# Optimization experiments

Measured on AMD Instinct MI355X. Metric: run time of the kernel, lower is better.

Reference implementation:

```python
import jax, jax.numpy as jnp
import numpy as np


def setup_inputs() -> dict:
    key = jax.random.key(0)
    B, H = 8192, 32768
    x = jax.random.normal(key, (B, H), dtype=jnp.float32)
    return {"hidden_preactivation_BH": x, "k": 64}


def reference(hidden_preactivation_BH, k):
    # top-k along last dim, then scatter values back into a zero tensor
    vals_BK, idx_BK = jax.lax.top_k(hidden_preactivation_BH, k)
    B = hidden_preactivation_BH.shape[0]
    rows_B1 = jnp.arange(B)[:, None]
    out_BH = jnp.zeros_like(hidden_preactivation_BH)
    out_BH = out_BH.at[rows_B1, idx_BK].set(vals_BK)
    return out_BH
```

## Files before the change

### kernel.cpp

```cpp
#include <hip/hip_runtime.h>
#include <stdint.h>

#define TPB 1024
#define NJ 8
#define HSZ 32768
#define NW (TPB / 64)
#define CAP 2048

__device__ __forceinline__ uint32_t f2k(float f) {
    uint32_t u = __float_as_uint(f);
    return u ^ (0x80000000u | (uint32_t)(-(int32_t)(u >> 31)));
}
__device__ __forceinline__ float k2f(uint32_t key) {
    uint32_t u = (key & 0x80000000u) ? (key ^ 0x80000000u) : ~key;
    return __uint_as_float(u);
}

__device__ __forceinline__ void select4096(const uint32_t* hist, uint32_t need,
                                           uint32_t* wtot, uint32_t* sh_bin,
                                           uint32_t* sh_rem, int t) {
    const int lane = t & 63, wid = t >> 6;
    uint32_t b[4], pt = 0;
#pragma unroll
    for (int jj = 0; jj < 4; ++jj) { b[jj] = hist[t * 4 + jj]; pt += b[jj]; }
    uint32_t pre = pt;
#pragma unroll
    for (int off = 1; off < 64; off <<= 1) {
        uint32_t n = (uint32_t)__shfl_down((int)pre, off, 64);
        if (lane + off < 64) pre += n;
    }
    if (lane == 0) wtot[wid] = pre;
    __syncthreads();
    uint32_t wsuf = 0;
    for (int w = wid + 1; w < NW; ++w) wsuf += wtot[w];
    const uint32_t Sincl = pre + wsuf;
    const uint32_t Sexcl = Sincl - pt;
    if (Sexcl < need && Sincl >= need) {
        uint32_t run = Sexcl;
#pragma unroll
        for (int jj = 3; jj >= 0; --jj) {
            if (run + b[jj] >= need) { *sh_bin = (uint32_t)(t * 4 + jj); *sh_rem = need - run; break; }
            run += b[jj];
        }
    }
    __syncthreads();
}

__device__ __forceinline__ void select256(const uint32_t* hist, uint32_t need,
                                          uint32_t* wtot, uint32_t* sh_bin,
                                          uint32_t* sh_rem, uint32_t* sh_eqcnt, int t) {
    const int lane = t & 63, wid = t >> 6;
    uint32_t pt = (t < 256) ? hist[t] : 0u;
    uint32_t pre = pt;
#pragma unroll
    for (int off = 1; off < 64; off <<= 1) {
        uint32_t n = (uint32_t)__shfl_down((int)pre, off, 64);
        if (lane + off < 64) pre += n;
    }
    if (lane == 0) wtot[wid] = pre;
    __syncthreads();
    uint32_t wsuf = 0;
    for (int w = wid + 1; w < NW; ++w) wsuf += wtot[w];
    const uint32_t Sincl = pre + wsuf;
    const uint32_t Sexcl = Sincl - pt;
    if (t < 256 && Sexcl < need && Sincl >= need) {
        *sh_bin = (uint32_t)t; *sh_rem = need - Sexcl; *sh_eqcnt = pt;
    }
    __syncthreads();
}

__global__ __launch_bounds__(TPB, 4) void topk_scatter_kernel(
    const float* __restrict__ x,
    const int* __restrict__ kp,
    float* __restrict__ out)
{
    __shared__ uint32_t hist[4096];
    __shared__ uint32_t wtot[NW];
    __shared__ uint32_t cand_key[CAP];
    __shared__ uint32_t cand_col[CAP];
    __shared__ uint32_t sh_bin, sh_rem, sh_eqcnt, sh_ncand;
    __shared__ uint32_t chunk_base;

    const int t = threadIdx.x;
    const size_t row = blockIdx.x;
    const float4* xr4 = reinterpret_cast<const float4*>(x + row * (size_t)HSZ);
    float* outr = out + row * (size_t)HSZ;
    float4* outr4 = reinterpret_cast<float4*>(outr);
    const uint32_t k = (uint32_t)kp[0];

    if (k == 0u || k >= (uint32_t)HSZ) {
#pragma unroll
        for (int j = 0; j < NJ; ++j) {
            float4 o;
            if (k == 0u) { o.x = o.y = o.z = o.w = 0.0f; }
            else o = xr4[j * TPB + t];
            outr4[j * TPB + t] = o;
        }
        return;
    }

    float4 vv[NJ];
#pragma unroll
    for (int j = 0; j < NJ; ++j) vv[j] = xr4[j * TPB + t];

    for (int i = t; i < 4096; i += TPB) hist[i] = 0u;
    if (t == 0) sh_ncand = 0u;
    __syncthreads();
#pragma unroll
    for (int j = 0; j < NJ; ++j) {
        atomicAdd(&hist[f2k(vv[j].x) >> 20], 1u);
        atomicAdd(&hist[f2k(vv[j].y) >> 20], 1u);
        atomicAdd(&hist[f2k(vv[j].z) >> 20], 1u);
        atomicAdd(&hist[f2k(vv[j].w) >> 20], 1u);
    }
    __syncthreads();
    select4096(hist, k, wtot, &sh_bin, &sh_rem, t);
    const uint32_t B1 = sh_bin;
    const uint32_t need2 = sh_rem;

#pragma unroll
    for (int j = 0; j < NJ; ++j) {
        float vals[4] = { vv[j].x, vv[j].y, vv[j].z, vv[j].w };
        float ov[4];
#pragma unroll
        for (int c = 0; c < 4; ++c) {
            uint32_t key = f2k(vals[c]);
            uint32_t b = key >> 20;
            ov[c] = (b > B1) ? vals[c] : 0.0f;
            if (b == B1) {
                uint32_t pos = atomicAdd(&sh_ncand, 1u);
                if (pos < CAP) {
                    cand_key[pos] = key;
                    cand_col[pos] = (uint32_t)((j * TPB + t) * 4 + c);
                }
            }
        }
        float4 o; o.x = ov[0]; o.y = ov[1]; o.z = ov[2]; o.w = ov[3];
        outr4[j * TPB + t] = o;
    }
    __syncthreads();
    const uint32_t C = sh_ncand;

    if (C <= CAP) {
        for (int i = t; i < 4096; i += TPB) hist[i] = 0u;
        __syncthreads();
        for (uint32_t i = t; i < C; i += TPB)
            atomicAdd(&hist[(cand_key[i] >> 8) & 0xFFFu], 1u);
        __syncthreads();
        select4096(hist, need2, wtot, &sh_bin, &sh_rem, t);
        const uint32_t B2 = sh_bin;
        const uint32_t need3 = sh_rem;

        if (t < 256) hist[t] = 0u;
        __syncthreads();
        const uint32_t pref = (B1 << 12) | B2;
        for (uint32_t i = t; i < C; i += TPB)
            if ((cand_key[i] >> 8) == pref) atomicAdd(&hist[cand_key[i] & 0xFFu], 1u);
        __syncthreads();
        select256(hist, need3, wtot, &sh_bin, &sh_rem, &sh_eqcnt, t);
        const uint32_t K = (pref << 8) | sh_bin;
        const uint32_t eqneed = sh_rem;
        const uint32_t eqcnt = sh_eqcnt;

        for (uint32_t i = t; i < C; i += TPB) {
            uint32_t key = cand_key[i];
            if (key > K) {
                outr[cand_col[i]] = k2f(key);
            } else if (key == K) {
                if (eqcnt == eqneed) {
                    outr[cand_col[i]] = k2f(key);
                } else {
                    uint32_t rank = 0, col = cand_col[i];
                    for (uint32_t m = 0; m < C; ++m)
                        if (cand_key[m] == K && cand_col[m] < col) ++rank;
                    if (rank < eqneed) outr[cand_col[i]] = k2f(key);
                }
            }
        }
    } else {
        for (int i = t; i < 4096; i += TPB) hist[i] = 0u;
        __syncthreads();
#pragma unroll
        for (int j = 0; j < NJ; ++j) {
            float vals[4] = { vv[j].x, vv[j].y, vv[j].z, vv[j].w };
#pragma unroll
            for (int c = 0; c < 4; ++c) {
                uint32_t key = f2k(vals[c]);
                if ((key >> 20) == B1) atomicAdd(&hist[(key >> 8) & 0xFFFu], 1u);
            }
        }
        __syncthreads();
        select4096(hist, need2, wtot, &sh_bin, &sh_rem, t);
        const uint32_t B2 = sh_bin;
        const uint32_t need3 = sh_rem;

        if (t < 256) hist[t] = 0u;
        __syncthreads();
        const uint32_t pref = (B1 << 12) | B2;
#pragma unroll
        for (int j = 0; j < NJ; ++j) {
            float vals[4] = { vv[j].x, vv[j].y, vv[j].z, vv[j].w };
#pragma unroll
            for (int c = 0; c < 4; ++c) {
                uint32_t key = f2k(vals[c]);
                if ((key >> 8) == pref) atomicAdd(&hist[key & 0xFFu], 1u);
            }
        }
        __syncthreads();
        select256(hist, need3, wtot, &sh_bin, &sh_rem, &sh_eqcnt, t);
        const uint32_t K = (pref << 8) | sh_bin;
        const uint32_t eqneed = sh_rem;
        const uint32_t eqcnt = sh_eqcnt;

        if (eqcnt == eqneed) {
#pragma unroll
            for (int j = 0; j < NJ; ++j) {
                float vals[4] = { vv[j].x, vv[j].y, vv[j].z, vv[j].w };
                float ov[4];
#pragma unroll
                for (int c = 0; c < 4; ++c)
                    ov[c] = (f2k(vals[c]) >= K) ? vals[c] : 0.0f;
                float4 o; o.x = ov[0]; o.y = ov[1]; o.z = ov[2]; o.w = ov[3];
                outr4[j * TPB + t] = o;
            }
        } else {
            if (t == 0) chunk_base = 0u;
            __syncthreads();
            const int lane = t & 63;
            const int wid = t >> 6;
            for (int j = 0; j < NJ; ++j) {
                float vals[4] = { vv[j].x, vv[j].y, vv[j].z, vv[j].w };
                uint32_t keys[4];
                uint32_t e = 0;
#pragma unroll
                for (int c = 0; c < 4; ++c) { keys[c] = f2k(vals[c]); e += (keys[c] == K) ? 1u : 0u; }
                uint32_t pre = e;
                for (int off = 1; off < 64; off <<= 1) {
                    uint32_t n = (uint32_t)__shfl_up((int)pre, off, 64);
                    if (lane >= off) pre += n;
                }
                if (lane == 63) wtot[wid] = pre;
                __syncthreads();
                uint32_t before = chunk_base + (pre - e);
                for (int w = 0; w < wid; ++w) before += wtot[w];
                float ov[4];
#pragma unroll
                for (int c = 0; c < 4; ++c) {
                    bool take = keys[c] > K;
                    if (keys[c] == K) { take = (before < eqneed); ++before; }
                    ov[c] = take ? vals[c] : 0.0f;
                }
                float4 o; o.x = ov[0]; o.y = ov[1]; o.z = ov[2]; o.w = ov[3];
                outr4[j * TPB + t] = o;
                __syncthreads();
                if (t == 0) {
                    uint32_t s2 = chunk_base;
#pragma unroll
                    for (int w = 0; w < NW; ++w) s2 += wtot[w];
                    chunk_base = s2;
                }
                __syncthreads();
            }
        }
    }
}

extern "C" void kernel_launch(void* const* d_in, const int* in_sizes, int n_in,
                              void* d_out, int out_size, void* d_ws, size_t ws_size,
                              hipStream_t stream) {
    const float* x = (const float*)d_in[0];
    const int* kp = (const int*)d_in[1];
    float* out = (float*)d_out;
    const int total = in_sizes[0];
    const int rows = total / HSZ;
    topk_scatter_kernel<<<rows, TPB, 0, stream>>>(x, kp, out);
}
```

Before: 465.6 us.

## Persistent blocks with register double-buffered row prefetch and lighter barriers

Switches to a persistent grid of at most 256 blocks, each looping over rows and prefetching the next row into a second register buffer while the current row is processed. Replaces __syncthreads with a custom LDS-wait plus s_barrier and halves the candidate buffer capacity. The aim is to hide global-load latency behind the histogram and select work, and to cut LDS footprint. In exchange it doubles register use for the row buffers, which can lower occupancy or cause spills, and 256 blocks may underfill the GPU. The smaller CAP also sends more rows down the slower fallback path.

```diff
diff --git a/kernel.cpp b/kernel.cpp
--- a/kernel.cpp
+++ b/kernel.cpp
@@ -5,7 +5,12 @@
 #define NJ 8
 #define HSZ 32768
 #define NW (TPB / 64)
-#define CAP 2048
+#define CAP 1024
+
+#define BARRIER() do { \
+    asm volatile("s_waitcnt lgkmcnt(0)" ::: "memory"); \
+    __builtin_amdgcn_s_barrier(); \
+} while (0)
 
 __device__ __forceinline__ uint32_t f2k(float f) {
     uint32_t u = __float_as_uint(f);
@@ -16,107 +21,89 @@
     return __uint_as_float(u);
 }
 
-__device__ __forceinline__ void select4096(const uint32_t* hist, uint32_t need,
-                                           uint32_t* wtot, uint32_t* sh_bin,
-                                           uint32_t* sh_rem, int t) {
+struct Sm {
+    uint32_t hist[4096];
+    uint32_t wtot[NW];
+    uint32_t cand_key[CAP];
+    uint32_t cand_col[CAP];
+    uint32_t bin, rem, eqcnt, ncand, chunk_base;
+};
+
+__device__ __forceinline__ void select4096(Sm& sm, uint32_t need, int t) {
     const int lane = t & 63, wid = t >> 6;
     uint32_t b[4], pt = 0;
 #pragma unroll
-    for (int jj = 0; jj < 4; ++jj) { b[jj] = hist[t * 4 + jj]; pt += b[jj]; }
+    for (int jj = 0; jj < 4; ++jj) { b[jj] = sm.hist[t * 4 + jj]; pt += b[jj]; }
     uint32_t pre = pt;
 #pragma unroll
     for (int off = 1; off < 64; off <<= 1) {
         uint32_t n = (uint32_t)__shfl_down((int)pre, off, 64);
         if (lane + off < 64) pre += n;
     }
-    if (lane == 0) wtot[wid] = pre;
-    __syncthreads();
+    if (lane == 0) sm.wtot[wid] = pre;
+    BARRIER();
     uint32_t wsuf = 0;
-    for (int w = wid + 1; w < NW; ++w) wsuf += wtot[w];
+    for (int w = wid + 1; w < NW; ++w) wsuf += sm.wtot[w];
     const uint32_t Sincl = pre + wsuf;
     const uint32_t Sexcl = Sincl - pt;
     if (Sexcl < need && Sincl >= need) {
         uint32_t run = Sexcl;
 #pragma unroll
         for (int jj = 3; jj >= 0; --jj) {
-            if (run + b[jj] >= need) { *sh_bin = (uint32_t)(t * 4 + jj); *sh_rem = need - run; break; }
+            if (run + b[jj] >= need) { sm.bin = (uint32_t)(t * 4 + jj); sm.rem = need - run; break; }
             run += b[jj];
         }
     }
-    __syncthreads();
-}
-
-__device__ __forceinline__ void select256(const uint32_t* hist, uint32_t need,
-                                          uint32_t* wtot, uint32_t* sh_bin,
-                                          uint32_t* sh_rem, uint32_t* sh_eqcnt, int t) {
+    BARRIER();
+}
+
+__device__ __forceinline__ void select256(Sm& sm, uint32_t need, int t) {
     const int lane = t & 63, wid = t >> 6;
-    uint32_t pt = (t < 256) ? hist[t] : 0u;
+    uint32_t pt = (t < 256) ? sm.hist[t] : 0u;
     uint32_t pre = pt;
 #pragma unroll
     for (int off = 1; off < 64; off <<= 1) {
         uint32_t n = (uint32_t)__shfl_down((int)pre, off, 64);
         if (lane + off < 64) pre += n;
     }
-    if (lane == 0) wtot[wid] = pre;
-    __syncthreads();
+    if (lane == 0) sm.wtot[wid] = pre;
+    BARRIER();
     uint32_t wsuf = 0;
-    for (int w = wid + 1; w < NW; ++w) wsuf += wtot[w];
+    for (int w = wid + 1; w < NW; ++w) wsuf += sm.wtot[w];
     const uint32_t Sincl = pre + wsuf;
     const uint32_t Sexcl = Sincl - pt;
     if (t < 256 && Sexcl < need && Sincl >= need) {
-        *sh_bin = (uint32_t)t; *sh_rem = need - Sexcl; *sh_eqcnt = pt;
-    }
-    __syncthreads();
-}
-
-__global__ __launch_bounds__(TPB, 4) void topk_scatter_kernel(
-    const float* __restrict__ x,
-    const int* __restrict__ kp,
-    float* __restrict__ out)
-{
-    __shared__ uint32_t hist[4096];
-    __shared__ uint32_t wtot[NW];
-    __shared__ uint32_t cand_key[CAP];
-    __shared__ uint32_t cand_col[CAP];
-    __shared__ uint32_t sh_bin, sh_rem, sh_eqcnt, sh_ncand;
-    __shared__ uint32_t chunk_base;
-
-    const int t = threadIdx.x;
-    const size_t row = blockIdx.x;
-    const float4* xr4 = reinterpret_cast<const float4*>(x + row * (size_t)HSZ);
-    float* outr = out + row * (size_t)HSZ;
+        sm.bin = (uint32_t)t; sm.rem = need - Sexcl; sm.eqcnt = pt;
+    }
+    BARRIER();
+}
+
+__device__ __forceinline__ void load_row(float4 (&dst)[NJ], const float* __restrict__ x,
+                                         int r, int t) {
+    const float4* p = reinterpret_cast<const float4*>(x + (size_t)r * HSZ);
+#pragma unroll
+    for (int j = 0; j < NJ; ++j) dst[j] = p[j * TPB + t];
+}
+
+__device__ __forceinline__ void process_row(const float4 (&vv)[NJ], float* __restrict__ outr,
+                                            uint32_t k, Sm& sm, int t) {
     float4* outr4 = reinterpret_cast<float4*>(outr);
-    const uint32_t k = (uint32_t)kp[0];
-
-    if (k == 0u || k >= (uint32_t)HSZ) {
-#pragma unroll
-        for (int j = 0; j < NJ; ++j) {
-            float4 o;
-            if (k == 0u) { o.x = o.y = o.z = o.w = 0.0f; }
-            else o = xr4[j * TPB + t];
-            outr4[j * TPB + t] = o;
-        }
-        return;
-    }
-
-    float4 vv[NJ];
-#pragma unroll
-    for (int j = 0; j < NJ; ++j) vv[j] = xr4[j * TPB + t];
-
-    for (int i = t; i < 4096; i += TPB) hist[i] = 0u;
-    if (t == 0) sh_ncand = 0u;
-    __syncthreads();
+
+#pragma unroll
+    for (int i = 0; i < 4096 / TPB; ++i) sm.hist[i * TPB + t] = 0u;
+    if (t == 0) sm.ncand = 0u;
+    BARRIER();
 #pragma unroll
     for (int j = 0; j < NJ; ++j) {
-        atomicAdd(&hist[f2k(vv[j].x) >> 20], 1u);
-        atomicAdd(&hist[f2k(vv[j].y) >> 20], 1u);
-        atomicAdd(&hist[f2k(vv[j].z) >> 20], 1u);
-        atomicAdd(&hist[f2k(vv[j].w) >> 20], 1u);
-    }
-    __syncthreads();
-    select4096(hist, k, wtot, &sh_bin, &sh_rem, t);
-    const uint32_t B1 = sh_bin;
-    const uint32_t need2 = sh_rem;
+        atomicAdd(&sm.hist[f2k(vv[j].x) >> 20], 1u);
+        atomicAdd(&sm.hist[f2k(vv[j].y) >> 20], 1u);
+        atomicAdd(&sm.hist[f2k(vv[j].z) >> 20], 1u);
+        atomicAdd(&sm.hist[f2k(vv[j].w) >> 20], 1u);
+    }
+    BARRIER();
+    select4096(sm, k, t);
+    const uint32_t B1 = sm.bin;
+    const uint32_t need2 = sm.rem;
 
 #pragma unroll
     for (int j = 0; j < NJ; ++j) {
@@ -128,74 +115,76 @@
             uint32_t b = key >> 20;
             ov[c] = (b > B1) ? vals[c] : 0.0f;
             if (b == B1) {
-                uint32_t pos = atomicAdd(&sh_ncand, 1u);
+                uint32_t pos = atomicAdd(&sm.ncand, 1u);
                 if (pos < CAP) {
-                    cand_key[pos] = key;
-                    cand_col[pos] = (uint32_t)((j * TPB + t) * 4 + c);
+                    sm.cand_key[pos] = key;
+                    sm.cand_col[pos] = (uint32_t)((j * TPB + t) * 4 + c);
                 }
             }
         }
         float4 o; o.x = ov[0]; o.y = ov[1]; o.z = ov[2]; o.w = ov[3];
         outr4[j * TPB + t] = o;
     }
-    __syncthreads();
-    const uint32_t C = sh_ncand;
+    BARRIER();
+    const uint32_t C = sm.ncand;
 
     if (C <= CAP) {
-        for (int i = t; i < 4096; i += TPB) hist[i] = 0u;
-        __syncthreads();
+#pragma unroll
+        for (int i = 0; i < 4096 / TPB; ++i) sm.hist[i * TPB + t] = 0u;
+        BARRIER();
         for (uint32_t i = t; i < C; i += TPB)
-            atomicAdd(&hist[(cand_key[i] >> 8) & 0xFFFu], 1u);
-        __syncthreads();
-        select4096(hist, need2, wtot, &sh_bin, &sh_rem, t);
-        const uint32_t B2 = sh_bin;
-        const uint32_t need3 = sh_rem;
-
-        if (t < 256) hist[t] = 0u;
-        __syncthreads();
+            atomicAdd(&sm.hist[(sm.cand_key[i] >> 8) & 0xFFFu], 1u);
+        BARRIER();
+        select4096(sm, need2, t);
+        const uint32_t B2 = sm.bin;
+        const uint32_t need3 = sm.rem;
+
+        if (t < 256) sm.hist[t] = 0u;
+        BARRIER();
         const uint32_t pref = (B1 << 12) | B2;
         for (uint32_t i = t; i < C; i += TPB)
-            if ((cand_key[i] >> 8) == pref) atomicAdd(&hist[cand_key[i] & 0xFFu], 1u);
-        __syncthreads();
-        select256(hist, need3, wtot, &sh_bin, &sh_rem, &sh_eqcnt, t);
-        const uint32_t K = (pref << 8) | sh_bin;
-        const uint32_t eqneed = sh_rem;
-        const uint32_t eqcnt = sh_eqcnt;
+            if ((sm.cand_key[i] >> 8) == pref) atomicAdd(&sm.hist[sm.cand_key[i] & 0xFFu], 1u);
+        BARRIER();
+        select256(sm, need3, t);
+        const uint32_t K = (pref << 8) | sm.bin;
+        const uint32_t eqneed = sm.rem;
+        const uint32_t eqcnt = sm.eqcnt;
 
         for (uint32_t i = t; i < C; i += TPB) {
-            uint32_t key = cand_key[i];
+            uint32_t key = sm.cand_key[i];
             if (key > K) {
-                outr[cand_col[i]] = k2f(key);
+                outr[sm.cand_col[i]] = k2f(key);
             } else if (key == K) {
                 if (eqcnt == eqneed) {
-                    outr[cand_col[i]] = k2f(key);
+                    outr[sm.cand_col[i]] = k2f(key);
                 } else {
-                    uint32_t rank = 0, col = cand_col[i];
+                    uint32_t rank = 0, col = sm.cand_col[i];
                     for (uint32_t m = 0; m < C; ++m)
-                        if (cand_key[m] == K && cand_col[m] < col) ++rank;
-                    if (rank < eqneed) outr[cand_col[i]] = k2f(key);
+                        if (sm.cand_key[m] == K && sm.cand_col[m] < col) ++rank;
+                    if (rank < eqneed) outr[sm.cand_col[i]] = k2f(key);
                 }
             }
         }
     } else {
-        for (int i = t; i < 4096; i += TPB) hist[i] = 0u;
-        __syncthreads();
+#pragma unroll
+        for (int i = 0; i < 4096 / TPB; ++i) sm.hist[i * TPB + t] = 0u;
+        BARRIER();
 #pragma unroll
         for (int j = 0; j < NJ; ++j) {
             float vals[4] = { vv[j].x, vv[j].y, vv[j].z, vv[j].w };
 #pragma unroll
             for (int c = 0; c < 4; ++c) {
                 uint32_t key = f2k(vals[c]);
-                if ((key >> 20) == B1) atomicAdd(&hist[(key >> 8) & 0xFFFu], 1u);
-            }
-        }
-        __syncthreads();
-        select4096(hist, need2, wtot, &sh_bin, &sh_rem, t);
-        const uint32_t B2 = sh_bin;
-        const uint32_t need3 = sh_rem;
-
-        if (t < 256) hist[t] = 0u;
-        __syncthreads();
+                if ((key >> 20) == B1) atomicAdd(&sm.hist[(key >> 8) & 0xFFFu], 1u);
+            }
+        }
+        BARRIER();
+        select4096(sm, need2, t);
+        const uint32_t B2 = sm.bin;
+        const uint32_t need3 = sm.rem;
+
+        if (t < 256) sm.hist[t] = 0u;
+        BARRIER();
         const uint32_t pref = (B1 << 12) | B2;
 #pragma unroll
         for (int j = 0; j < NJ; ++j) {
@@ -203,14 +192,14 @@
 #pragma unroll
             for (int c = 0; c < 4; ++c) {
                 uint32_t key = f2k(vals[c]);
-                if ((key >> 8) == pref) atomicAdd(&hist[key & 0xFFu], 1u);
-            }
-        }
-        __syncthreads();
-        select256(hist, need3, wtot, &sh_bin, &sh_rem, &sh_eqcnt, t);
-        const uint32_t K = (pref << 8) | sh_bin;
-        const uint32_t eqneed = sh_rem;
-        const uint32_t eqcnt = sh_eqcnt;
+                if ((key >> 8) == pref) atomicAdd(&sm.hist[key & 0xFFu], 1u);
+            }
+        }
+        BARRIER();
+        select256(sm, need3, t);
+        const uint32_t K = (pref << 8) | sm.bin;
+        const uint32_t eqneed = sm.rem;
+        const uint32_t eqcnt = sm.eqcnt;
 
         if (eqcnt == eqneed) {
 #pragma unroll
@@ -224,8 +213,8 @@
                 outr4[j * TPB + t] = o;
             }
         } else {
-            if (t == 0) chunk_base = 0u;
-            __syncthreads();
+            if (t == 0) sm.chunk_base = 0u;
+            BARRIER();
             const int lane = t & 63;
             const int wid = t >> 6;
             for (int j = 0; j < NJ; ++j) {
@@ -239,10 +228,10 @@
                     uint32_t n = (uint32_t)__shfl_up((int)pre, off, 64);
                     if (lane >= off) pre += n;
                 }
-                if (lane == 63) wtot[wid] = pre;
-                __syncthreads();
-                uint32_t before = chunk_base + (pre - e);
-                for (int w = 0; w < wid; ++w) before += wtot[w];
+                if (lane == 63) sm.wtot[wid] = pre;
+                BARRIER();
+                uint32_t before = sm.chunk_base + (pre - e);
+                for (int w = 0; w < wid; ++w) before += sm.wtot[w];
                 float ov[4];
 #pragma unroll
                 for (int c = 0; c < 4; ++c) {
@@ -252,16 +241,60 @@
                 }
                 float4 o; o.x = ov[0]; o.y = ov[1]; o.z = ov[2]; o.w = ov[3];
                 outr4[j * TPB + t] = o;
-                __syncthreads();
+                BARRIER();
                 if (t == 0) {
-                    uint32_t s2 = chunk_base;
-#pragma unroll
-                    for (int w = 0; w < NW; ++w) s2 += wtot[w];
-                    chunk_base = s2;
-                }
-                __syncthreads();
-            }
-        }
+                    uint32_t s2 = sm.chunk_base;
+#pragma unroll
+                    for (int w = 0; w < NW; ++w) s2 += sm.wtot[w];
+                    sm.chunk_base = s2;
+                }
+                BARRIER();
+            }
+        }
+    }
+}
+
+__global__ __launch_bounds__(TPB, 4) void topk_scatter_kernel(
+    const float* __restrict__ x,
+    const int* __restrict__ kp,
+    float* __restrict__ out,
+    int nrows)
+{
+    __shared__ Sm sm;
+    const int t = threadIdx.x;
+    const uint32_t k = (uint32_t)kp[0];
+    const int gs = (int)gridDim.x;
+
+    if (k == 0u || k >= (uint32_t)HSZ) {
+        for (int r = (int)blockIdx.x; r < nrows; r += gs) {
+            const float4* xr4 = reinterpret_cast<const float4*>(x + (size_t)r * HSZ);
+            float4* outr4 = reinterpret_cast<float4*>(out + (size_t)r * HSZ);
+#pragma unroll
+            for (int j = 0; j < NJ; ++j) {
+                float4 o;
+                if (k == 0u) { o.x = o.y = o.z = o.w = 0.0f; }
+                else o = xr4[j * TPB + t];
+                outr4[j * TPB + t] = o;
+            }
+        }
+        return;
+    }
+
+    int r = (int)blockIdx.x;
+    if (r >= nrows) return;
+    float4 va[NJ], vb[NJ];
+    load_row(va, x, r, t);
+    for (;;) {
+        const int rB = r + gs;
+        if (rB < nrows) load_row(vb, x, rB, t);
+        process_row(va, out + (size_t)r * HSZ, k, sm, t);
+        if (rB >= nrows) return;
+
+        const int rC = rB + gs;
+        if (rC < nrows) load_row(va, x, rC, t);
+        process_row(vb, out + (size_t)rB * HSZ, k, sm, t);
+        if (rC >= nrows) return;
+        r = rC;
     }
 }
 
@@ -273,5 +306,6 @@
     float* out = (float*)d_out;
     const int total = in_sizes[0];
     const int rows = total / HSZ;
-    topk_scatter_kernel<<<rows, TPB, 0, stream>>>(x, kp, out);
-}
+    int grid = rows < 256 ? rows : 256;
+    topk_scatter_kernel<<<grid, TPB, 0, stream>>>(x, kp, out, rows);
+}
```

Result: slower. 956.7 us (+105.5%).
